# Kernel optimization log

Hardware: AMD Instinct MI355X
Metric: run time of the kernel (lower is better)

## Reference

```python
import jax, jax.numpy as jnp
import numpy as np
import math

FEATURES = 1024; HEADS = 8; STATES = 64; DCONV = 4; EXPAND = 2; NGROUPS = 1; CHUNK = 256
INNER = EXPAND * FEATURES           # 2048
HALF = INNER // 2                   # 1024
HEADDIM = HALF // HEADS             # 128
CONVDIM = HALF + 2 * NGROUPS * STATES  # 1152
B = 2; L = 4096
EPS = 1e-5


def setup_inputs() -> dict:
    key = jax.random.key(0)
    ks = jax.random.split(key, 8)
    u = jax.random.normal(ks[0], (B, L, FEATURES), jnp.float32)
    W_in = jax.random.normal(ks[1], (FEATURES, INNER + 2 * NGROUPS * STATES + HEADS), jnp.float32) * (FEATURES ** -0.5)
    xconv_w = jax.random.normal(ks[2], (CONVDIM, DCONV), jnp.float32) * (DCONV ** -0.5)
    xconv_b = jnp.zeros((CONVDIM,), jnp.float32)
    zconv_w = jax.random.normal(ks[3], (HALF, DCONV), jnp.float32) * (DCONV ** -0.5)
    zconv_b = jnp.zeros((HALF,), jnp.float32)
    dt0 = jnp.exp(jax.random.uniform(ks[4], (HEADS,)) * (math.log(0.1) - math.log(0.001)) + math.log(0.001))
    dt0 = jnp.clip(dt0, 1e-4, None)
    dt_bias = dt0 + jnp.log(-jnp.expm1(-dt0))  # inverse-softplus init
    Alog = jnp.log(jax.random.uniform(ks[5], (HEADS,), minval=1.0, maxval=16.0))
    D = jnp.ones((HEADS,), jnp.float32)
    norm_w = jnp.ones((INNER,), jnp.float32)
    W_out = jax.random.normal(ks[6], (INNER, FEATURES), jnp.float32) * (INNER ** -0.5)
    return dict(u=u, W_in=W_in, xconv_w=xconv_w, xconv_b=xconv_b, zconv_w=zconv_w,
                zconv_b=zconv_b, dt_bias=dt_bias, Alog=Alog, D=D, norm_w=norm_w, W_out=W_out)


def _causal_dwconv_silu(x, w, b):
    # x: (B, L, C), w: (C, K) depthwise, b: (C,) -> causal conv + SiLU, (B, L, C)
    xt = jnp.transpose(x, (0, 2, 1))  # B C L
    kern = w[:, None, :]              # (C, 1, K) -> OIH with groups=C
    y = jax.lax.conv_general_dilated(xt, kern, window_strides=(1,),
                                     padding=[(w.shape[1] - 1, 0)],
                                     dimension_numbers=('NCH', 'OIH', 'NCH'),
                                     feature_group_count=w.shape[0])
    y = jax.nn.silu(y + b[None, :, None])
    return jnp.transpose(y, (0, 2, 1))


def _ssd(x, dt, A, Bm, Cm, Dp, chunk):
    # x:(b,l,h,p) dt:(b,l,h) A:(h,) Bm,Cm:(b,l,g,n) Dp:(h,)
    b, Ltot, H, P = x.shape
    G, N = Bm.shape[2], Bm.shape[3]
    nc = Ltot // chunk
    X = (x * dt[..., None]).reshape(b, nc, chunk, H, P)          # dt-scaled input
    Adt = jnp.transpose((dt * A[None, None, :]).reshape(b, nc, chunk, H), (0, 3, 1, 2))  # b h c k
    Bh = jnp.repeat(Bm, H // G, axis=2).reshape(b, nc, chunk, H, N)
    Ch = jnp.repeat(Cm, H // G, axis=2).reshape(b, nc, chunk, H, N)
    cs = jnp.cumsum(Adt, axis=-1)                                # b h c k
    seg = cs[..., :, None] - cs[..., None, :]                    # b h c l s
    mask = jnp.tril(jnp.ones((chunk, chunk), bool))
    Lmat = jnp.exp(jnp.where(mask, seg, -jnp.inf))               # causal decay matrix
    # intra-chunk (diagonal block) output
    Y_diag = jnp.einsum('bclhn,bcshn,bhcls,bcshp->bclhp', Ch, Bh, Lmat, X)
    # per-chunk final states
    decay_states = jnp.exp(cs[..., -1:] - cs)                    # b h c k
    states = jnp.einsum('bcshn,bhcs,bcshp->bchpn', Bh, decay_states, X)
    chunk_decay = jnp.exp(cs[..., -1])                           # b h c
    def step(carry, inp):
        s, d = inp
        return s + d[..., None, None] * carry, carry             # emit incoming state
    _, prev = jax.lax.scan(step, jnp.zeros((b, H, P, N), x.dtype),
                           (jnp.transpose(states, (1, 0, 2, 3, 4)),
                            jnp.transpose(chunk_decay, (2, 0, 1))))  # prev: (c,b,h,p,n)
    Y_off = jnp.einsum('bclhn,bhcl,cbhpn->bclhp', Ch, jnp.exp(cs), prev)
    Y = (Y_diag + Y_off).reshape(b, Ltot, H, P)
    return Y + Dp[None, None, :, None] * x                       # D skip uses raw x


def _forward(u, W_in, xconv_w, xconv_b, zconv_w, zconv_b, dt_bias, Alog, D, norm_w, W_out):
    zxbcdt = u @ W_in
    z = zxbcdt[..., :HALF]
    xBC = zxbcdt[..., HALF:HALF + CONVDIM]
    dt = jax.nn.softplus(zxbcdt[..., HALF + CONVDIM:] + dt_bias)  # (B,L,H)
    A = -jnp.exp(Alog)
    xBC = _causal_dwconv_silu(xBC, xconv_w, xconv_b)
    z = _causal_dwconv_silu(z, zconv_w, zconv_b)
    x = xBC[..., :HALF].reshape(B, L, HEADS, HEADDIM)
    Bm = xBC[..., HALF:HALF + NGROUPS * STATES].reshape(B, L, NGROUPS, STATES)
    Cm = xBC[..., HALF + NGROUPS * STATES:].reshape(B, L, NGROUPS, STATES)
    y = _ssd(x, dt, A, Bm, Cm, D, CHUNK).reshape(B, L, HALF)
    y = jnp.concatenate([y, z], axis=-1)                          # (B,L,INNER)
    y = y * jax.lax.rsqrt(jnp.mean(y * y, axis=-1, keepdims=True) + EPS) * norm_w
    return y @ W_out


def reference(u, W_in, xconv_w, xconv_b, zconv_w, zconv_b, dt_bias, Alog, D, norm_w, W_out):
    return _forward(u, W_in, xconv_w, xconv_b, zconv_w, zconv_b, dt_bias, Alog, D, norm_w, W_out)
```

## Files before the change

kernel.cpp:

```cpp
#include <hip/hip_runtime.h>
#include <stdint.h>

#define DEV __device__ __forceinline__

typedef __attribute__((ext_vector_type(8))) short bf16x8_t;
typedef __attribute__((ext_vector_type(4))) float f32x4_t;

DEV unsigned short f2bf(float f) {
  union { float f; uint32_t u; } x; x.f = f;
  uint32_t r = x.u + 0x7fffu + ((x.u >> 16) & 1u);
  return (unsigned short)(r >> 16);
}
DEV float bf2f(unsigned short u) {
  union { uint32_t u; float f; } x; x.u = ((uint32_t)u) << 16;
  return x.f;
}

#define GLOAD_LDS16(g, l)                                                              \
  __builtin_amdgcn_global_load_lds((const __attribute__((address_space(1))) unsigned int*)(g), \
                                   (__attribute__((address_space(3))) unsigned int*)(l), 16, 0, 0)

__global__ __launch_bounds__(256) void wdt_kernel(const float* __restrict__ W_in, float* __restrict__ Wdt) {
  int k = blockIdx.x * 256 + threadIdx.x;
  if (k < 1024) {
#pragma unroll
    for (int h = 0; h < 8; ++h)
      Wdt[h * 1024 + k] = W_in[(size_t)k * 2184 + 2176 + h];
  }
}

__global__ __launch_bounds__(256) void uin_kernel(const float* __restrict__ u, const float* __restrict__ Wdt,
                                                  const float* __restrict__ dt_bias,
                                                  unsigned short* __restrict__ A1, float* __restrict__ dtv) {
  int tid = threadIdx.x;
  int row0 = blockIdx.x * 4;
  int lane = tid & 63, wv = tid >> 6;
  float4 w4[8];
#pragma unroll
  for (int h = 0; h < 8; ++h) w4[h] = reinterpret_cast<const float4*>(Wdt + h * 1024)[tid];
  __shared__ float red[4][8];
#pragma unroll
  for (int r = 0; r < 4; ++r) {
    int row = row0 + r;
    float4 v = reinterpret_cast<const float4*>(u + (size_t)row * 1024)[tid];
    ushort4 o;
    o.x = f2bf(v.x); o.y = f2bf(v.y); o.z = f2bf(v.z); o.w = f2bf(v.w);
    reinterpret_cast<ushort4*>(A1 + (size_t)row * 1024)[tid] = o;
    float ps[8];
#pragma unroll
    for (int h = 0; h < 8; ++h)
      ps[h] = v.x * w4[h].x + v.y * w4[h].y + v.z * w4[h].z + v.w * w4[h].w;
#pragma unroll
    for (int h = 0; h < 8; ++h)
#pragma unroll
      for (int off = 32; off > 0; off >>= 1) ps[h] += __shfl_down(ps[h], off, 64);
    if (lane == 0) {
#pragma unroll
      for (int h = 0; h < 8; ++h) red[wv][h] = ps[h];
    }
    __syncthreads();
    if (tid < 8) {
      float s = red[0][tid] + red[1][tid] + red[2][tid] + red[3][tid] + dt_bias[tid];
      float sp = (s > 20.f) ? s : log1pf(expf(s));
      dtv[(size_t)row * 8 + tid] = sp;
    }
    __syncthreads();
  }
}

__global__ void transpose_bf16_kernel(const float* __restrict__ in, unsigned short* __restrict__ out,
                                      int R, int Cin, int stride) {
  __shared__ float t[32][33];
  int bx = blockIdx.x, by = blockIdx.y;
  int tx = threadIdx.x, ty = threadIdx.y;
#pragma unroll
  for (int q = 0; q < 4; ++q) {
    int r = by * 32 + ty + q * 8, c = bx * 32 + tx;
    t[ty + q * 8][tx] = (c < Cin) ? in[(size_t)r * stride + c] : 0.f;
  }
  __syncthreads();
#pragma unroll
  for (int q = 0; q < 4; ++q) {
    int oc = bx * 32 + ty + q * 8;
    int orr = by * 32 + tx;
    out[(size_t)oc * R + orr] = f2bf(t[tx][ty + q * 8]);
  }
}

template <int OBF>
__global__ __launch_bounds__(512) void gemm_tb_kernel(const unsigned short* __restrict__ A,
                                                      const unsigned short* __restrict__ Bt,
                                                      void* __restrict__ Cout, int K, int ldc, int gx) {
  __shared__ __align__(16) char lds[3 * 24576];
  int tid = threadIdx.x, lane = tid & 63, wv = tid >> 6;
  int lr = lane & 15, lk = lane >> 4;
  int wm = wv >> 2, wn = wv & 3;

  int nwg = gridDim.x, lin = blockIdx.x, wg = lin;
  if ((nwg & 7) == 0) { int cpx = nwg >> 3; wg = (lin & 7) * cpx + (lin >> 3); }
  long tileM = (long)(wg % gx) * 128;
  long tileN = (long)(wg / gx) * 256;

  const unsigned short* gAp;
  {
    int q = tid, row = q >> 2, c = (q & 3) ^ ((row >> 1) & 3);
    gAp = A + (size_t)(tileM + row) * K + c * 8;
  }
  const unsigned short* gBp[2];
#pragma unroll
  for (int i = 0; i < 2; ++i) {
    int q = tid + i * 512, row = q >> 2, c = (q & 3) ^ ((row >> 1) & 3);
    gBp[i] = Bt + (size_t)(tileN + row) * K + c * 8;
  }

#define STAGE_TB(bsel, kof)                                                                  \
  do {                                                                                       \
    GLOAD_LDS16(gAp + (kof), lds + (bsel) * 24576 + tid * 16);                               \
    _Pragma("unroll") for (int i_ = 0; i_ < 2; ++i_)                                         \
        GLOAD_LDS16(gBp[i_] + (kof), lds + (bsel) * 24576 + 8192 + (tid + i_ * 512) * 16);   \
  } while (0)

  f32x4_t acc[4][4];
#pragma unroll
  for (int i = 0; i < 4; ++i)
#pragma unroll
    for (int j = 0; j < 4; ++j) acc[i][j] = f32x4_t{0.f, 0.f, 0.f, 0.f};

  int NT = K >> 5;
  STAGE_TB(0, 0);
  STAGE_TB(1, 32);

  int colsw = ((lk ^ ((lr >> 1) & 3)) << 4);
  int rsel = 0, wsel = 2;
  for (int t = 0; t < NT; ++t) {
    __builtin_amdgcn_s_barrier();
    if (t + 2 < NT) {
      STAGE_TB(wsel, (t + 2) * 32);
      asm volatile("s_waitcnt vmcnt(6)" ::: "memory");
    } else if (t + 1 < NT) {
      asm volatile("s_waitcnt vmcnt(3)" ::: "memory");
    } else {
      asm volatile("s_waitcnt vmcnt(0)" ::: "memory");
    }
    __builtin_amdgcn_s_barrier();

    const char* base = lds + rsel * 24576;
    bf16x8_t a[4], b[4];
#pragma unroll
    for (int mf = 0; mf < 4; ++mf)
      a[mf] = *reinterpret_cast<const bf16x8_t*>(base + (wm * 64 + mf * 16 + lr) * 64 + colsw);
#pragma unroll
    for (int nf = 0; nf < 4; ++nf)
      b[nf] = *reinterpret_cast<const bf16x8_t*>(base + 8192 + (wn * 64 + nf * 16 + lr) * 64 + colsw);
    __builtin_amdgcn_s_setprio(1);
#pragma unroll
    for (int mf = 0; mf < 4; ++mf)
#pragma unroll
      for (int nf = 0; nf < 4; ++nf)
        acc[mf][nf] = __builtin_amdgcn_mfma_f32_16x16x32_bf16(a[mf], b[nf], acc[mf][nf], 0, 0, 0);
    __builtin_amdgcn_s_setprio(0);
    rsel = (rsel == 2) ? 0 : rsel + 1;
    wsel = (wsel == 2) ? 0 : wsel + 1;
  }
#undef STAGE_TB

#pragma unroll
  for (int mf = 0; mf < 4; ++mf)
#pragma unroll
    for (int nf = 0; nf < 4; ++nf) {
      long r0 = tileM + wm * 64 + mf * 16 + lk * 4;
      long c0 = tileN + wn * 64 + nf * 16 + lr;
#pragma unroll
      for (int r = 0; r < 4; ++r) {
        if (OBF)
          ((unsigned short*)Cout)[(size_t)(r0 + r) * ldc + c0] = f2bf(acc[mf][nf][r]);
        else
          ((float*)Cout)[(size_t)(r0 + r) * ldc + c0] = acc[mf][nf][r];
      }
    }
}

template <int C, int IN_STRIDE>
__global__ __launch_bounds__(256) void conv_silu_tile_kernel(const unsigned short* __restrict__ in,
                                                             const float* __restrict__ w,
                                                             const float* __restrict__ bias,
                                                             unsigned short* __restrict__ outp) {
  constexpr int CG = C / 8;
  int idx = blockIdx.x * 256 + threadIdx.x;
  int ch_grp = idx % CG;
  int tb = idx / CG;
  int t0 = (tb & 511) * 8;
  int b = tb >> 9;
  int ch0 = ch_grp * 8;

  float4 wv[8];
#pragma unroll
  for (int e = 0; e < 8; ++e) wv[e] = *reinterpret_cast<const float4*>(w + (ch0 + e) * 4);
  float bs[8];
  {
    float4 b0 = *reinterpret_cast<const float4*>(bias + ch0);
    float4 b1 = *reinterpret_cast<const float4*>(bias + ch0 + 4);
    bs[0] = b0.x; bs[1] = b0.y; bs[2] = b0.z; bs[3] = b0.w;
    bs[4] = b1.x; bs[5] = b1.y; bs[6] = b1.z; bs[7] = b1.w;
  }

  float rows[11][8];
#pragma unroll
  for (int k = 0; k < 11; ++k) {
    int t = t0 - 3 + k;
    if (t >= 0) {
      bf16x8_t v = *reinterpret_cast<const bf16x8_t*>(in + (size_t)((b << 12) + t) * IN_STRIDE + ch0);
#pragma unroll
      for (int e = 0; e < 8; ++e) rows[k][e] = bf2f((unsigned short)v[e]);
    } else {
#pragma unroll
      for (int e = 0; e < 8; ++e) rows[k][e] = 0.f;
    }
  }

#pragma unroll
  for (int tp = 0; tp < 8; ++tp) {
    bf16x8_t o;
#pragma unroll
    for (int e = 0; e < 8; ++e) {
      float a = bs[e] + wv[e].x * rows[tp][e] + wv[e].y * rows[tp + 1][e] +
                wv[e].z * rows[tp + 2][e] + wv[e].w * rows[tp + 3][e];
      a = a / (1.f + expf(-a));
      o[e] = (short)f2bf(a);
    }
    *reinterpret_cast<bf16x8_t*>(outp + (size_t)((b << 12) + t0 + tp) * C + ch0) = o;
  }
}

__global__ __launch_bounds__(256) void ssd1_kernel(const unsigned short* __restrict__ xBC,
                                                   const float* __restrict__ dtv,
                                                   const float* __restrict__ Alog,
                                                   float* __restrict__ csb,
                                                   unsigned short* __restrict__ stat,
                                                   unsigned short* __restrict__ ypart) {
  int blk = blockIdx.x;
  int h = blk & 7, bc = blk >> 3;
  int c = bc & 63, b = bc >> 6;
  int tid = threadIdx.x, lane = tid & 63, wv = tid >> 6;
  int lr = lane & 15, lk = lane >> 4;
  int base = b * 4096 + c * 64;

  __shared__ float csc[64], dts[64], ew[64];
  __shared__ __align__(16) unsigned short Xd[128 * 72];
  __shared__ __align__(16) unsigned short Bnj[64 * 72];
  __shared__ __align__(16) unsigned short Ss[64 * 72];

  if (wv == 0) {
    int j = lane;
    float dt = dtv[(size_t)(base + j) * 8 + h];
    float A = -expf(Alog[h]);
    float s = dt * A;
#pragma unroll
    for (int off = 1; off < 64; off <<= 1) {
      float v = __shfl_up(s, off, 64);
      if (lane >= off) s += v;
    }
    float csl = __shfl(s, 63, 64);
    csc[j] = s; dts[j] = dt; ew[j] = expf(csl - s);
    csb[(size_t)blk * 64 + j] = s;
  }
  __syncthreads();

#pragma unroll
  for (int rr = 0; rr < 4; ++rr) {
    int j = rr * 16 + (tid >> 4);
    int pc = tid & 15;
    bf16x8_t v = *reinterpret_cast<const bf16x8_t*>(xBC + (size_t)(base + j) * 1152 + h * 128 + pc * 8);
    float dj = dts[j];
    int js = j ^ ((pc & 7) << 3);
#pragma unroll
    for (int e = 0; e < 8; ++e) {
      int p = pc * 8 + e;
      Xd[p * 72 + js] = f2bf(bf2f((unsigned short)v[e]) * dj);
    }
  }
#pragma unroll
  for (int rr = 0; rr < 2; ++rr) {
    int j = rr * 32 + (tid >> 3);
    int nc = tid & 7;
    bf16x8_t v = *reinterpret_cast<const bf16x8_t*>(xBC + (size_t)(base + j) * 1152 + 1024 + nc * 8);
    int js = j ^ ((nc & 7) << 3);
#pragma unroll
    for (int e = 0; e < 8; ++e) {
      int n = nc * 8 + e;
      Bnj[n * 72 + js] = (unsigned short)v[e];
    }
  }

  bf16x8_t cf[2];
  {
    size_t crow = (size_t)(base + wv * 16 + lr) * 1152 + 1088;
    cf[0] = *reinterpret_cast<const bf16x8_t*>(xBC + crow + lk * 8);
    cf[1] = *reinterpret_cast<const bf16x8_t*>(xBC + crow + 32 + lk * 8);
  }
  f32x4_t sacc[4];
#pragma unroll
  for (int jf = 0; jf < 4; ++jf) sacc[jf] = f32x4_t{0.f, 0.f, 0.f, 0.f};
#pragma unroll
  for (int ks = 0; ks < 2; ++ks) {
#pragma unroll
    for (int jf = 0; jf < 4; ++jf) {
      bf16x8_t bv = *reinterpret_cast<const bf16x8_t*>(
          xBC + (size_t)(base + jf * 16 + lr) * 1152 + 1024 + ks * 32 + lk * 8);
      sacc[jf] = __builtin_amdgcn_mfma_f32_16x16x32_bf16(cf[ks], bv, sacc[jf], 0, 0, 0);
    }
  }
  __syncthreads();

  {
    float csi[4];
#pragma unroll
    for (int r = 0; r < 4; ++r) csi[r] = csc[wv * 16 + lk * 4 + r];
#pragma unroll
    for (int jf = 0; jf < 4; ++jf) {
      int j = jf * 16 + lr;
      float csj = csc[j];
#pragma unroll
      for (int r = 0; r < 4; ++r) {
        int i = wv * 16 + lk * 4 + r;
        float w = (j <= i) ? expf(csi[r] - csj) : 0.f;
        Ss[i * 72 + j] = f2bf(sacc[jf][r] * w);
      }
    }
  }
  __syncthreads();

  f32x4_t yacc[8];
#pragma unroll
  for (int pf = 0; pf < 8; ++pf) yacc[pf] = f32x4_t{0.f, 0.f, 0.f, 0.f};
  bf16x8_t sa[2];
  sa[0] = *reinterpret_cast<const bf16x8_t*>(Ss + (wv * 16 + lr) * 72 + lk * 8);
  sa[1] = *reinterpret_cast<const bf16x8_t*>(Ss + (wv * 16 + lr) * 72 + 32 + lk * 8);
#pragma unroll
  for (int ks = 0; ks < 2; ++ks) {
    int jb = ks * 32 + lk * 8;
#pragma unroll
    for (int pf = 0; pf < 8; ++pf) {
      int p = pf * 16 + lr;
      bf16x8_t xv = *reinterpret_cast<const bf16x8_t*>(Xd + p * 72 + (jb ^ (((p >> 3) & 7) << 3)));
      yacc[pf] = __builtin_amdgcn_mfma_f32_16x16x32_bf16(sa[ks], xv, yacc[pf], 0, 0, 0);
    }
  }

  f32x4_t st[2][4];
#pragma unroll
  for (int pb = 0; pb < 2; ++pb)
#pragma unroll
    for (int nf = 0; nf < 4; ++nf) st[pb][nf] = f32x4_t{0.f, 0.f, 0.f, 0.f};
#pragma unroll
  for (int pb = 0; pb < 2; ++pb) {
    int p = wv * 32 + pb * 16 + lr;
#pragma unroll
    for (int ks = 0; ks < 2; ++ks) {
      int jb = ks * 32 + lk * 8;
      bf16x8_t xv = *reinterpret_cast<const bf16x8_t*>(Xd + p * 72 + (jb ^ (((p >> 3) & 7) << 3)));
      bf16x8_t xs;
#pragma unroll
      for (int e = 0; e < 8; ++e) xs[e] = (short)f2bf(bf2f((unsigned short)xv[e]) * ew[jb + e]);
#pragma unroll
      for (int nf = 0; nf < 4; ++nf) {
        int n = nf * 16 + lr;
        bf16x8_t bv = *reinterpret_cast<const bf16x8_t*>(Bnj + n * 72 + (jb ^ (((n >> 3) & 7) << 3)));
        st[pb][nf] = __builtin_amdgcn_mfma_f32_16x16x32_bf16(xs, bv, st[pb][nf], 0, 0, 0);
      }
    }
  }

#pragma unroll
  for (int pf = 0; pf < 8; ++pf)
#pragma unroll
    for (int r = 0; r < 4; ++r) {
      int i = wv * 16 + lk * 4 + r;
      ypart[(size_t)(base + i) * 1024 + h * 128 + pf * 16 + lr] = f2bf(yacc[pf][r]);
    }
  unsigned short* so = stat + (size_t)blk * 8192;
#pragma unroll
  for (int pb = 0; pb < 2; ++pb)
#pragma unroll
    for (int nf = 0; nf < 4; ++nf)
#pragma unroll
      for (int r = 0; r < 4; ++r)
        so[(size_t)(wv * 32 + pb * 16 + lk * 4 + r) * 64 + nf * 16 + lr] = f2bf(st[pb][nf][r]);
}

__global__ __launch_bounds__(256) void scan_kernel(const unsigned short* __restrict__ stat,
                                                   const float* __restrict__ csb,
                                                   unsigned short* __restrict__ prevb) {
  int bh = blockIdx.x >> 5;
  int part = blockIdx.x & 31;
  int h = bh & 7, b = bh >> 3;
  int e = part * 256 + threadIdx.x;
  float carry = 0.f;
  for (int c = 0; c < 64; ++c) {
    size_t blk = (size_t)(b * 64 + c) * 8 + h;
    size_t idx = blk * 8192 + e;
    prevb[idx] = f2bf(carry);
    float dec = expf(csb[blk * 64 + 63]);
    carry = bf2f(stat[idx]) + dec * carry;
  }
}

__global__ __launch_bounds__(256) void ssd2_kernel(const unsigned short* __restrict__ xBC,
                                                   const float* __restrict__ csb,
                                                   const unsigned short* __restrict__ prevb,
                                                   const float* __restrict__ Dp,
                                                   const unsigned short* __restrict__ ypart,
                                                   unsigned short* __restrict__ yb) {
  int blk = blockIdx.x;
  int h = blk & 7, bc = blk >> 3;
  int c = bc & 63, b = bc >> 6;
  int tid = threadIdx.x, lane = tid & 63, wv = tid >> 6;
  int lr = lane & 15, lk = lane >> 4;
  int base = b * 4096 + c * 64;
  __shared__ float csc[64];
  if (tid < 64) csc[tid] = csb[(size_t)blk * 64 + tid];
  __syncthreads();

  float sc = expf(csc[wv * 16 + lr]);
  bf16x8_t ca[2];
  {
    size_t crow = (size_t)(base + wv * 16 + lr) * 1152 + 1088;
#pragma unroll
    for (int ks = 0; ks < 2; ++ks) {
      bf16x8_t v = *reinterpret_cast<const bf16x8_t*>(xBC + crow + ks * 32 + lk * 8);
      bf16x8_t d;
#pragma unroll
      for (int e = 0; e < 8; ++e) d[e] = (short)f2bf(bf2f((unsigned short)v[e]) * sc);
      ca[ks] = d;
    }
  }
  f32x4_t acc[8];
#pragma unroll
  for (int pf = 0; pf < 8; ++pf) acc[pf] = f32x4_t{0.f, 0.f, 0.f, 0.f};
#pragma unroll
  for (int ks = 0; ks < 2; ++ks) {
#pragma unroll
    for (int pf = 0; pf < 8; ++pf) {
      bf16x8_t pv = *reinterpret_cast<const bf16x8_t*>(
          prevb + (size_t)blk * 8192 + (size_t)(pf * 16 + lr) * 64 + ks * 32 + lk * 8);
      acc[pf] = __builtin_amdgcn_mfma_f32_16x16x32_bf16(ca[ks], pv, acc[pf], 0, 0, 0);
    }
  }
  float Dh = Dp[h];
#pragma unroll
  for (int pf = 0; pf < 8; ++pf)
#pragma unroll
    for (int r = 0; r < 4; ++r) {
      int i = wv * 16 + lk * 4 + r;
      size_t row = (size_t)(base + i);
      int p = pf * 16 + lr;
      float xr = bf2f(xBC[row * 1152 + h * 128 + p]);
      float yv = bf2f(ypart[row * 1024 + h * 128 + p]) + acc[pf][r] + Dh * xr;
      yb[row * 1024 + h * 128 + p] = f2bf(yv);
    }
}

__global__ __launch_bounds__(256) void rmsnorm_kernel(const unsigned short* __restrict__ y,
                                                      const unsigned short* __restrict__ z,
                                                      const float* __restrict__ nw,
                                                      unsigned short* __restrict__ out) {
  int row = blockIdx.x, tid = threadIdx.x;
  ushort4 ya = reinterpret_cast<const ushort4*>(y + (size_t)row * 1024)[tid];
  ushort4 za = reinterpret_cast<const ushort4*>(z + (size_t)row * 1024)[tid];
  float yf[4] = {bf2f(ya.x), bf2f(ya.y), bf2f(ya.z), bf2f(ya.w)};
  float zf[4] = {bf2f(za.x), bf2f(za.y), bf2f(za.z), bf2f(za.w)};
  float ss = yf[0] * yf[0] + yf[1] * yf[1] + yf[2] * yf[2] + yf[3] * yf[3] +
             zf[0] * zf[0] + zf[1] * zf[1] + zf[2] * zf[2] + zf[3] * zf[3];
#pragma unroll
  for (int off = 32; off > 0; off >>= 1) ss += __shfl_down(ss, off, 64);
  __shared__ float red[4];
  __shared__ float stot;
  int lane = tid & 63, wv = tid >> 6;
  if (lane == 0) red[wv] = ss;
  __syncthreads();
  if (tid == 0) stot = rsqrtf((red[0] + red[1] + red[2] + red[3]) * (1.f / 2048.f) + 1e-5f);
  __syncthreads();
  float s = stot;
  float4 w1 = reinterpret_cast<const float4*>(nw)[tid];
  float4 w2 = reinterpret_cast<const float4*>(nw + 1024)[tid];
  ushort4 o1, o2;
  o1.x = f2bf(yf[0] * s * w1.x); o1.y = f2bf(yf[1] * s * w1.y);
  o1.z = f2bf(yf[2] * s * w1.z); o1.w = f2bf(yf[3] * s * w1.w);
  o2.x = f2bf(zf[0] * s * w2.x); o2.y = f2bf(zf[1] * s * w2.y);
  o2.z = f2bf(zf[2] * s * w2.z); o2.w = f2bf(zf[3] * s * w2.w);
  reinterpret_cast<ushort4*>(out + (size_t)row * 2048)[tid] = o1;
  reinterpret_cast<ushort4*>(out + (size_t)row * 2048 + 1024)[tid] = o2;
}

extern "C" void kernel_launch(void* const* d_in, const int* in_sizes, int n_in,
                              void* d_out, int out_size, void* d_ws, size_t ws_size,
                              hipStream_t stream) {
  const float* u       = (const float*)d_in[0];
  const float* W_in    = (const float*)d_in[1];
  const float* xconv_w = (const float*)d_in[2];
  const float* xconv_b = (const float*)d_in[3];
  const float* zconv_w = (const float*)d_in[4];
  const float* zconv_b = (const float*)d_in[5];
  const float* dt_bias = (const float*)d_in[6];
  const float* Alog    = (const float*)d_in[7];
  const float* Dp      = (const float*)d_in[8];
  const float* norm_w  = (const float*)d_in[9];
  const float* W_out   = (const float*)d_in[10];
  float* out = (float*)d_out;

  char* ws = (char*)d_ws;
  size_t o = 0;
  auto alc = [&](size_t bytes) { void* p = (void*)(ws + o); o = (o + bytes + 255) & ~(size_t)255; return p; };
  char* regA = (char*)alc(16777216);
  unsigned short* Wt1    = (unsigned short*)alc(4718592);
  unsigned short* Wt2    = (unsigned short*)alc(4194304);
  char* regZ = (char*)alc(37748736);
  float*          dtv    = (float*)alc(262144);
  float*          csb    = (float*)alc(262144);
  unsigned short* xBC    = (unsigned short*)alc(18874368);
  unsigned short* zc     = (unsigned short*)alc(16777216);
  char* regS = (char*)alc(33554432);
  unsigned short* prevb  = (unsigned short*)alc(16777216);
  float*          Wdt    = (float*)alc(32768);
  (void)ws_size; (void)in_sizes; (void)n_in; (void)out_size;

  unsigned short* A1     = (unsigned short*)regA;
  unsigned short* yb     = (unsigned short*)regA;
  unsigned short* zx     = (unsigned short*)regZ;
  unsigned short* ypart  = (unsigned short*)regZ;
  unsigned short* stat   = (unsigned short*)regS;
  unsigned short* normed = (unsigned short*)regS;

  dim3 tb(32, 8);
  wdt_kernel<<<4, 256, 0, stream>>>(W_in, Wdt);
  uin_kernel<<<2048, 256, 0, stream>>>(u, Wdt, dt_bias, A1, dtv);
  transpose_bf16_kernel<<<dim3(72, 32), tb, 0, stream>>>(W_in, Wt1, 1024, 2176, 2184);
  transpose_bf16_kernel<<<dim3(32, 64), tb, 0, stream>>>(W_out, Wt2, 2048, 1024, 1024);
  gemm_tb_kernel<1><<<576, 512, 0, stream>>>(A1, Wt1, (void*)zx, 1024, 2304, 64);
  conv_silu_tile_kernel<1152, 2304><<<576, 256, 0, stream>>>(zx + 1024, xconv_w, xconv_b, xBC);
  conv_silu_tile_kernel<1024, 2304><<<512, 256, 0, stream>>>(zx, zconv_w, zconv_b, zc);
  ssd1_kernel<<<1024, 256, 0, stream>>>(xBC, dtv, Alog, csb, stat, ypart);
  scan_kernel<<<512, 256, 0, stream>>>(stat, csb, prevb);
  ssd2_kernel<<<1024, 256, 0, stream>>>(xBC, csb, prevb, Dp, ypart, yb);
  rmsnorm_kernel<<<8192, 256, 0, stream>>>(yb, zc, norm_w, normed);
  gemm_tb_kernel<0><<<256, 512, 0, stream>>>(normed, Wt2, (void*)out, 2048, 1024, 64);
}
```

Before: 222.1 us.

## Fuse z causal depthwise conv and SiLU into the RMSNorm kernel

Removes the separate conv_silu launch for the z branch. The RMSNorm kernel now reads four time-shifted rows of the raw z projection, applies the depthwise conv and SiLU in registers, and then normalizes. This drops a full write and read of the conv output. It costs four strided reads per row, partly served by cache, and needs a new workspace layout so ypart no longer aliases zx, which must stay live until the norm.

Measured after the change: 229.9 us. 3.5% more time.

```diff
diff --git a/kernel.cpp b/kernel.cpp
--- a/kernel.cpp
+++ b/kernel.cpp
@@ -460,15 +460,42 @@
     }
 }
 
-__global__ __launch_bounds__(256) void rmsnorm_kernel(const unsigned short* __restrict__ y,
-                                                      const unsigned short* __restrict__ z,
-                                                      const float* __restrict__ nw,
-                                                      unsigned short* __restrict__ out) {
+__global__ __launch_bounds__(256) void rmsnorm_zconv_kernel(const unsigned short* __restrict__ yb,
+                                                            const unsigned short* __restrict__ zx,
+                                                            const float* __restrict__ zw,
+                                                            const float* __restrict__ zbias,
+                                                            const float* __restrict__ nw,
+                                                            unsigned short* __restrict__ out) {
   int row = blockIdx.x, tid = threadIdx.x;
-  ushort4 ya = reinterpret_cast<const ushort4*>(y + (size_t)row * 1024)[tid];
-  ushort4 za = reinterpret_cast<const ushort4*>(z + (size_t)row * 1024)[tid];
+  int b = row >> 12, t = row & 4095;
+  int ch = tid * 4;
+
+  ushort4 ya = reinterpret_cast<const ushort4*>(yb + (size_t)row * 1024)[tid];
   float yf[4] = {bf2f(ya.x), bf2f(ya.y), bf2f(ya.z), bf2f(ya.w)};
-  float zf[4] = {bf2f(za.x), bf2f(za.y), bf2f(za.z), bf2f(za.w)};
+
+  float wk[4][4];
+#pragma unroll
+  for (int e = 0; e < 4; ++e) {
+    float4 t4 = *reinterpret_cast<const float4*>(zw + (ch + e) * 4);
+    wk[e][0] = t4.x; wk[e][1] = t4.y; wk[e][2] = t4.z; wk[e][3] = t4.w;
+  }
+  float4 bb = reinterpret_cast<const float4*>(zbias)[tid];
+  float za[4] = {bb.x, bb.y, bb.z, bb.w};
+#pragma unroll
+  for (int k = 0; k < 4; ++k) {
+    int tt = t - 3 + k;
+    if (tt >= 0) {
+      ushort4 zv = *reinterpret_cast<const ushort4*>(zx + (size_t)((b << 12) + tt) * 2304 + ch);
+      za[0] += bf2f(zv.x) * wk[0][k];
+      za[1] += bf2f(zv.y) * wk[1][k];
+      za[2] += bf2f(zv.z) * wk[2][k];
+      za[3] += bf2f(zv.w) * wk[3][k];
+    }
+  }
+  float zf[4];
+#pragma unroll
+  for (int e = 0; e < 4; ++e) zf[e] = za[e] / (1.f + expf(-za[e]));
+
   float ss = yf[0] * yf[0] + yf[1] * yf[1] + yf[2] * yf[2] + yf[3] * yf[3] +
              zf[0] * zf[0] + zf[1] * zf[1] + zf[2] * zf[2] + zf[3] * zf[3];
 #pragma unroll
@@ -514,11 +541,11 @@
   char* regA = (char*)alc(16777216);
   unsigned short* Wt1    = (unsigned short*)alc(4718592);
   unsigned short* Wt2    = (unsigned short*)alc(4194304);
-  char* regZ = (char*)alc(37748736);
+  unsigned short* zx     = (unsigned short*)alc(37748736);
   float*          dtv    = (float*)alc(262144);
   float*          csb    = (float*)alc(262144);
   unsigned short* xBC    = (unsigned short*)alc(18874368);
-  unsigned short* zc     = (unsigned short*)alc(16777216);
+  unsigned short* ypart  = (unsigned short*)alc(16777216);
   char* regS = (char*)alc(33554432);
   unsigned short* prevb  = (unsigned short*)alc(16777216);
   float*          Wdt    = (float*)alc(32768);
@@ -526,8 +553,6 @@
 
   unsigned short* A1     = (unsigned short*)regA;
   unsigned short* yb     = (unsigned short*)regA;
-  unsigned short* zx     = (unsigned short*)regZ;
-  unsigned short* ypart  = (unsigned short*)regZ;
   unsigned short* stat   = (unsigned short*)regS;
   unsigned short* normed = (unsigned short*)regS;
 
@@ -538,10 +563,9 @@
   transpose_bf16_kernel<<<dim3(32, 64), tb, 0, stream>>>(W_out, Wt2, 2048, 1024, 1024);
   gemm_tb_kernel<1><<<576, 512, 0, stream>>>(A1, Wt1, (void*)zx, 1024, 2304, 64);
   conv_silu_tile_kernel<1152, 2304><<<576, 256, 0, stream>>>(zx + 1024, xconv_w, xconv_b, xBC);
-  conv_silu_tile_kernel<1024, 2304><<<512, 256, 0, stream>>>(zx, zconv_w, zconv_b, zc);
   ssd1_kernel<<<1024, 256, 0, stream>>>(xBC, dtv, Alog, csb, stat, ypart);
   scan_kernel<<<512, 256, 0, stream>>>(stat, csb, prevb);
   ssd2_kernel<<<1024, 256, 0, stream>>>(xBC, csb, prevb, Dp, ypart, yb);
-  rmsnorm_kernel<<<8192, 256, 0, stream>>>(yb, zc, norm_w, normed);
+  rmsnorm_zconv_kernel<<<8192, 256, 0, stream>>>(yb, zx, zconv_w, zconv_b, norm_w, normed);
   gemm_tb_kernel<0><<<256, 512, 0, stream>>>(normed, Wt2, (void*)out, 2048, 1024, 64);
 }
```

## Fuse SSD inter-chunk output with RMSNorm via shared-memory row staging

Applied to the files above, without the earlier changes.

Merges the ssd2 kernel and the rmsnorm kernel into one kernel. Each 512-thread block handles 16 rows across all 8 heads, stages y in LDS, accumulates the sum of squares with shared atomics, then normalizes y and z and writes the normed output directly. This removes the yb round trip through global memory and one launch. In exchange it uses fewer blocks (512) and adds LDS atomics and barriers.

New measurement: 224.6 us. Within noise of the previous version (+1.1%).

```diff
diff --git a/kernel.cpp b/kernel.cpp
--- a/kernel.cpp
+++ b/kernel.cpp
@@ -405,26 +405,34 @@
   }
 }
 
-__global__ __launch_bounds__(256) void ssd2_kernel(const unsigned short* __restrict__ xBC,
-                                                   const float* __restrict__ csb,
-                                                   const unsigned short* __restrict__ prevb,
-                                                   const float* __restrict__ Dp,
-                                                   const unsigned short* __restrict__ ypart,
-                                                   unsigned short* __restrict__ yb) {
-  int blk = blockIdx.x;
-  int h = blk & 7, bc = blk >> 3;
-  int c = bc & 63, b = bc >> 6;
-  int tid = threadIdx.x, lane = tid & 63, wv = tid >> 6;
+__global__ __launch_bounds__(512) void ssd2_norm_kernel(const unsigned short* __restrict__ xBC,
+                                                        const float* __restrict__ csb,
+                                                        const unsigned short* __restrict__ prevb,
+                                                        const float* __restrict__ Dp,
+                                                        const unsigned short* __restrict__ ypart,
+                                                        const unsigned short* __restrict__ zc,
+                                                        const float* __restrict__ nw,
+                                                        unsigned short* __restrict__ out) {
+  __shared__ __align__(16) unsigned short ysm[16 * 1032];
+  __shared__ float ssq[16];
+  __shared__ float sfac[16];
+  int tid = threadIdx.x, lane = tid & 63, h = tid >> 6;
   int lr = lane & 15, lk = lane >> 4;
-  int base = b * 4096 + c * 64;
-  __shared__ float csc[64];
-  if (tid < 64) csc[tid] = csb[(size_t)blk * 64 + tid];
-  __syncthreads();
-
-  float sc = expf(csc[wv * 16 + lr]);
+  int R0 = blockIdx.x * 16;
+  int b = R0 >> 12;
+  int r4 = R0 & 4095;
+  int c = r4 >> 6;
+  int q0 = r4 & 63;
+  int blkh = (b * 64 + c) * 8 + h;
+
+  if (tid < 16) ssq[tid] = 0.f;
+  __syncthreads();
+
+  float Dh = Dp[h];
+  float sc = expf(csb[(size_t)blkh * 64 + q0 + lr]);
   bf16x8_t ca[2];
   {
-    size_t crow = (size_t)(base + wv * 16 + lr) * 1152 + 1088;
+    size_t crow = (size_t)(R0 + lr) * 1152 + 1088;
 #pragma unroll
     for (int ks = 0; ks < 2; ++ks) {
       bf16x8_t v = *reinterpret_cast<const bf16x8_t*>(xBC + crow + ks * 32 + lk * 8);
@@ -442,54 +450,75 @@
 #pragma unroll
     for (int pf = 0; pf < 8; ++pf) {
       bf16x8_t pv = *reinterpret_cast<const bf16x8_t*>(
-          prevb + (size_t)blk * 8192 + (size_t)(pf * 16 + lr) * 64 + ks * 32 + lk * 8);
+          prevb + (size_t)blkh * 8192 + (size_t)(pf * 16 + lr) * 64 + ks * 32 + lk * 8);
       acc[pf] = __builtin_amdgcn_mfma_f32_16x16x32_bf16(ca[ks], pv, acc[pf], 0, 0, 0);
     }
   }
-  float Dh = Dp[h];
-#pragma unroll
-  for (int pf = 0; pf < 8; ++pf)
-#pragma unroll
-    for (int r = 0; r < 4; ++r) {
-      int i = wv * 16 + lk * 4 + r;
-      size_t row = (size_t)(base + i);
+
+#pragma unroll
+  for (int r = 0; r < 4; ++r) {
+    int row = lk * 4 + r;
+    size_t R = (size_t)(R0 + row);
+    float partial = 0.f;
+#pragma unroll
+    for (int pf = 0; pf < 8; ++pf) {
       int p = pf * 16 + lr;
-      float xr = bf2f(xBC[row * 1152 + h * 128 + p]);
-      float yv = bf2f(ypart[row * 1024 + h * 128 + p]) + acc[pf][r] + Dh * xr;
-      yb[row * 1024 + h * 128 + p] = f2bf(yv);
-    }
-}
-
-__global__ __launch_bounds__(256) void rmsnorm_kernel(const unsigned short* __restrict__ y,
-                                                      const unsigned short* __restrict__ z,
-                                                      const float* __restrict__ nw,
-                                                      unsigned short* __restrict__ out) {
-  int row = blockIdx.x, tid = threadIdx.x;
-  ushort4 ya = reinterpret_cast<const ushort4*>(y + (size_t)row * 1024)[tid];
-  ushort4 za = reinterpret_cast<const ushort4*>(z + (size_t)row * 1024)[tid];
-  float yf[4] = {bf2f(ya.x), bf2f(ya.y), bf2f(ya.z), bf2f(ya.w)};
-  float zf[4] = {bf2f(za.x), bf2f(za.y), bf2f(za.z), bf2f(za.w)};
-  float ss = yf[0] * yf[0] + yf[1] * yf[1] + yf[2] * yf[2] + yf[3] * yf[3] +
-             zf[0] * zf[0] + zf[1] * zf[1] + zf[2] * zf[2] + zf[3] * zf[3];
-#pragma unroll
-  for (int off = 32; off > 0; off >>= 1) ss += __shfl_down(ss, off, 64);
-  __shared__ float red[4];
-  __shared__ float stot;
-  int lane = tid & 63, wv = tid >> 6;
-  if (lane == 0) red[wv] = ss;
-  __syncthreads();
-  if (tid == 0) stot = rsqrtf((red[0] + red[1] + red[2] + red[3]) * (1.f / 2048.f) + 1e-5f);
-  __syncthreads();
-  float s = stot;
-  float4 w1 = reinterpret_cast<const float4*>(nw)[tid];
-  float4 w2 = reinterpret_cast<const float4*>(nw + 1024)[tid];
-  ushort4 o1, o2;
-  o1.x = f2bf(yf[0] * s * w1.x); o1.y = f2bf(yf[1] * s * w1.y);
-  o1.z = f2bf(yf[2] * s * w1.z); o1.w = f2bf(yf[3] * s * w1.w);
-  o2.x = f2bf(zf[0] * s * w2.x); o2.y = f2bf(zf[1] * s * w2.y);
-  o2.z = f2bf(zf[2] * s * w2.z); o2.w = f2bf(zf[3] * s * w2.w);
-  reinterpret_cast<ushort4*>(out + (size_t)row * 2048)[tid] = o1;
-  reinterpret_cast<ushort4*>(out + (size_t)row * 2048 + 1024)[tid] = o2;
+      float xr = bf2f(xBC[R * 1152 + h * 128 + p]);
+      float yv = bf2f(ypart[R * 1024 + h * 128 + p]) + acc[pf][r] + Dh * xr;
+      partial += yv * yv;
+      ysm[row * 1032 + h * 128 + p] = f2bf(yv);
+    }
+#pragma unroll
+    for (int m = 1; m < 16; m <<= 1) partial += __shfl_xor(partial, m, 64);
+    if (lr == 0) atomicAdd(&ssq[row], partial);
+  }
+
+  int zr = tid >> 5, sub = tid & 31;
+  size_t Rz = (size_t)(R0 + zr);
+  bf16x8_t zv[4];
+  float zpart = 0.f;
+#pragma unroll
+  for (int k = 0; k < 4; ++k) {
+    zv[k] = *reinterpret_cast<const bf16x8_t*>(zc + Rz * 1024 + k * 256 + sub * 8);
+#pragma unroll
+    for (int e = 0; e < 8; ++e) { float z = bf2f((unsigned short)zv[k][e]); zpart += z * z; }
+  }
+  atomicAdd(&ssq[zr], zpart);
+  __syncthreads();
+  if (tid < 16) sfac[tid] = rsqrtf(ssq[tid] * (1.f / 2048.f) + 1e-5f);
+  __syncthreads();
+
+  float s = sfac[zr];
+#pragma unroll
+  for (int k = 0; k < 4; ++k) {
+    int col = k * 256 + sub * 8;
+    bf16x8_t y8 = *reinterpret_cast<const bf16x8_t*>(ysm + zr * 1032 + col);
+    float4 wy0 = *reinterpret_cast<const float4*>(nw + col);
+    float4 wy1 = *reinterpret_cast<const float4*>(nw + col + 4);
+    bf16x8_t oy;
+    oy[0] = (short)f2bf(bf2f((unsigned short)y8[0]) * s * wy0.x);
+    oy[1] = (short)f2bf(bf2f((unsigned short)y8[1]) * s * wy0.y);
+    oy[2] = (short)f2bf(bf2f((unsigned short)y8[2]) * s * wy0.z);
+    oy[3] = (short)f2bf(bf2f((unsigned short)y8[3]) * s * wy0.w);
+    oy[4] = (short)f2bf(bf2f((unsigned short)y8[4]) * s * wy1.x);
+    oy[5] = (short)f2bf(bf2f((unsigned short)y8[5]) * s * wy1.y);
+    oy[6] = (short)f2bf(bf2f((unsigned short)y8[6]) * s * wy1.z);
+    oy[7] = (short)f2bf(bf2f((unsigned short)y8[7]) * s * wy1.w);
+    *reinterpret_cast<bf16x8_t*>(out + Rz * 2048 + col) = oy;
+
+    float4 wz0 = *reinterpret_cast<const float4*>(nw + 1024 + col);
+    float4 wz1 = *reinterpret_cast<const float4*>(nw + 1024 + col + 4);
+    bf16x8_t oz;
+    oz[0] = (short)f2bf(bf2f((unsigned short)zv[k][0]) * s * wz0.x);
+    oz[1] = (short)f2bf(bf2f((unsigned short)zv[k][1]) * s * wz0.y);
+    oz[2] = (short)f2bf(bf2f((unsigned short)zv[k][2]) * s * wz0.z);
+    oz[3] = (short)f2bf(bf2f((unsigned short)zv[k][3]) * s * wz0.w);
+    oz[4] = (short)f2bf(bf2f((unsigned short)zv[k][4]) * s * wz1.x);
+    oz[5] = (short)f2bf(bf2f((unsigned short)zv[k][5]) * s * wz1.y);
+    oz[6] = (short)f2bf(bf2f((unsigned short)zv[k][6]) * s * wz1.z);
+    oz[7] = (short)f2bf(bf2f((unsigned short)zv[k][7]) * s * wz1.w);
+    *reinterpret_cast<bf16x8_t*>(out + Rz * 2048 + 1024 + col) = oz;
+  }
 }
 
 extern "C" void kernel_launch(void* const* d_in, const int* in_sizes, int n_in,
@@ -511,7 +540,7 @@
   char* ws = (char*)d_ws;
   size_t o = 0;
   auto alc = [&](size_t bytes) { void* p = (void*)(ws + o); o = (o + bytes + 255) & ~(size_t)255; return p; };
-  char* regA = (char*)alc(16777216);
+  unsigned short* A1     = (unsigned short*)alc(16777216);
   unsigned short* Wt1    = (unsigned short*)alc(4718592);
   unsigned short* Wt2    = (unsigned short*)alc(4194304);
   char* regZ = (char*)alc(37748736);
@@ -524,8 +553,6 @@
   float*          Wdt    = (float*)alc(32768);
   (void)ws_size; (void)in_sizes; (void)n_in; (void)out_size;
 
-  unsigned short* A1     = (unsigned short*)regA;
-  unsigned short* yb     = (unsigned short*)regA;
   unsigned short* zx     = (unsigned short*)regZ;
   unsigned short* ypart  = (unsigned short*)regZ;
   unsigned short* stat   = (unsigned short*)regS;
@@ -541,7 +568,6 @@
   conv_silu_tile_kernel<1024, 2304><<<512, 256, 0, stream>>>(zx, zconv_w, zconv_b, zc);
   ssd1_kernel<<<1024, 256, 0, stream>>>(xBC, dtv, Alog, csb, stat, ypart);
   scan_kernel<<<512, 256, 0, stream>>>(stat, csb, prevb);
-  ssd2_kernel<<<1024, 256, 0, stream>>>(xBC, csb, prevb, Dp, ypart, yb);
-  rmsnorm_kernel<<<8192, 256, 0, stream>>>(yb, zc, norm_w, normed);
+  ssd2_norm_kernel<<<512, 512, 0, stream>>>(xBC, csb, prevb, Dp, ypart, zc, norm_w, normed);
   gemm_tb_kernel<0><<<256, 512, 0, stream>>>(normed, Wt2, (void*)out, 2048, 1024, 64);
 }
```
